# Performance work log

Measured on AMD Instinct MI355X. Metric: run time of the kernel, lower is better.

Reference implementation:

```python
import jax, jax.numpy as jnp
import numpy as np

P, B, D, H, O = 512, 8, 256, 75, 128  # passage_len, batch, input_size, attn hidden, GRU hidden


def setup_inputs() -> dict:
    key = jax.random.key(0)
    ks = jax.random.split(key, 10)

    def w(k, shape, fan_in):
        return jax.random.normal(k, shape, jnp.float32) * (1.0 / np.sqrt(fan_in))

    return {
        "v": jax.random.normal(ks[0], (P, B, D), jnp.float32),
        "Wvp1": w(ks[1], (H, D), D),          # nn.Linear(input_size, hidden, bias=False)
        "Wvp2": w(ks[2], (H, D), D),
        "vw": w(ks[3], (H,), H),               # nn.Linear(hidden, 1, bias=False)
        "Wg": w(ks[4], (2 * D, 2 * D), 2 * D),  # Gate linear, no bias
        "w_ih_f": w(ks[5], (3 * O, 2 * D), 2 * D),
        "w_hh_f": w(ks[6], (3 * O, O), O),
        "b_ih_f": jnp.zeros((3 * O,), jnp.float32),
        "b_hh_f": jnp.zeros((3 * O,), jnp.float32),
        "w_ih_b": w(ks[7], (3 * O, 2 * D), 2 * D),
        "w_hh_b": w(ks[8], (3 * O, O), O),
        "b_ih_b": jnp.zeros((3 * O,), jnp.float32),
        "b_hh_b": jnp.zeros((3 * O,), jnp.float32),
    }


def _gru(x, w_ih, w_hh, b_ih, b_hh):
    # x: (T, B, in) -> hidden states (T, B, O); PyTorch GRU gate order (r, z, n)
    hdim = w_hh.shape[1]
    xp = x @ w_ih.T + b_ih  # precompute input projections: (T, B, 3O)

    def step(h, xp_t):
        gh = h @ w_hh.T + b_hh
        i_r, i_z, i_n = jnp.split(xp_t, 3, axis=-1)
        h_r, h_z, h_n = jnp.split(gh, 3, axis=-1)
        r = jax.nn.sigmoid(i_r + h_r)
        z = jax.nn.sigmoid(i_z + h_z)
        n = jnp.tanh(i_n + r * h_n)
        h_new = (1.0 - z) * n + z * h
        return h_new, h_new

    h0 = jnp.zeros((x.shape[1], hdim), x.dtype)
    _, hs = jax.lax.scan(step, h0, xp)
    return hs


def reference(v, Wvp1, Wvp2, vw, Wg,
              w_ih_f, w_hh_f, b_ih_f, b_hh_f,
              w_ih_b, w_hh_b, b_ih_b, b_hh_b):
    # dropout is inference no-op (and in the torch code its result is discarded anyway)
    Wv1 = v @ Wvp1.T  # (P, B, H) -- broadcast over key axis (dim 1 after expand)
    Wv2 = v @ Wvp2.T  # (P, B, H) -- broadcast over query axis
    # s[i, j, b, h] = tanh(Wv2[i] + Wv1[j]); softmax over i (keys)
    s = jnp.tanh(Wv2[:, None] + Wv1[None, :])          # (P, P, B, H)
    scores = jnp.einsum('ijbh,h->ijb', s, vw)          # (P, P, B)
    a = jax.nn.softmax(scores, axis=0)
    c = jnp.einsum('ijb,ibd->jbd', a, v)               # attended context (P, B, D)
    g = jnp.concatenate([v, c], axis=2)                # (P, B, 2D)
    g = jax.nn.sigmoid(g @ Wg.T) * g                   # Gate
    hf = _gru(g, w_ih_f, w_hh_f, b_ih_f, b_hh_f)
    hb = _gru(g[::-1], w_ih_b, w_hh_b, b_ih_b, b_hh_b)[::-1]
    return jnp.concatenate([hf, hb], axis=2)           # (P, B, 2O)
```

## Files before the change

### kernel.cpp

```cpp
#include <hip/hip_runtime.h>

#define TP 512
#define TB 8
#define TD 256
#define TH 75
#define THP 80
#define TO 128

typedef _Float16 half_t;
typedef _Float16 half2v __attribute__((ext_vector_type(2)));
typedef _Float16 half4v __attribute__((ext_vector_type(4)));
typedef _Float16 half8v __attribute__((ext_vector_type(8)));
typedef float    float4v __attribute__((ext_vector_type(4)));

__device__ __forceinline__ float fast_rcp(float x) { return __builtin_amdgcn_rcpf(x); }
__device__ __forceinline__ float fast_tanh(float x) {
    return 1.0f - 2.0f * fast_rcp(1.0f + __expf(2.0f * x));
}
__device__ __forceinline__ float fast_sigmoid(float x) {
    return fast_rcp(1.0f + __expf(-x));
}
__device__ __forceinline__ float fdot2h(half2v a, half2v b, float c) {
#if __has_builtin(__builtin_amdgcn_fdot2)
    return __builtin_amdgcn_fdot2(a, b, c, false);
#else
    return c + (float)a[0] * (float)b[0] + (float)a[1] * (float)b[1];
#endif
}
#define EXT2(v, j) __builtin_shufflevector((v), (v), 2*(j), 2*(j)+1)
__device__ __forceinline__ void dot3_h8(half8v wr, half8v wz, half8v wn, half8v h,
                                        float& ar, float& az, float& an) {
    half2v h0 = EXT2(h, 0), h1 = EXT2(h, 1), h2 = EXT2(h, 2), h3 = EXT2(h, 3);
    ar = fdot2h(EXT2(wr, 0), h0, ar);
    az = fdot2h(EXT2(wz, 0), h0, az);
    an = fdot2h(EXT2(wn, 0), h0, an);
    ar = fdot2h(EXT2(wr, 1), h1, ar);
    az = fdot2h(EXT2(wz, 1), h1, az);
    an = fdot2h(EXT2(wn, 1), h1, an);
    ar = fdot2h(EXT2(wr, 2), h2, ar);
    az = fdot2h(EXT2(wz, 2), h2, az);
    an = fdot2h(EXT2(wn, 2), h2, an);
    ar = fdot2h(EXT2(wr, 3), h3, ar);
    az = fdot2h(EXT2(wz, 3), h3, az);
    an = fdot2h(EXT2(wn, 3), h3, an);
}
__device__ __forceinline__ float pair_sum_dpp(float v) {
    int i1 = __builtin_amdgcn_update_dpp(0, __builtin_bit_cast(int, v), 0xB1, 0xF, 0xF, true);
    return v + __builtin_bit_cast(float, i1);
}

__global__ __launch_bounds__(256) void prep_kernel(
    const float* __restrict__ v,
    const float* __restrict__ Wvp1, const float* __restrict__ Wvp2,
    const float* __restrict__ Wg,   const float* __restrict__ wihf,
    const float* __restrict__ wihb, const float* __restrict__ bihf,
    const float* __restrict__ bihb, const float* __restrict__ whhf,
    const float* __restrict__ whhb,
    float* __restrict__ bihC,
    half_t* __restrict__ v16, half_t* __restrict__ g16,
    half_t* __restrict__ Wg16B, half_t* __restrict__ Wih16B,
    half_t* __restrict__ whh16, half_t* __restrict__ WT16B)
{
    int idx = blockIdx.x * 256 + threadIdx.x;
    if (idx < 1048576) {
        half_t val = (half_t)v[idx];
        v16[idx] = val;
        int row = idx >> 8, d = idx & 255;
        g16[row * 512 + d] = val;
        return;
    }
    idx -= 1048576;
    if (idx < 768) { bihC[idx] = (idx < 384) ? bihf[idx] : bihb[idx - 384]; return; }
    idx -= 768;
    if (idx < 262144) {
        int j = idx & 7, lane = (idx >> 3) & 63, kt = (idx >> 9) & 15, nt = idx >> 13;
        int o = nt * 16 + (lane & 15);
        int k = kt * 32 + ((lane >> 4) << 3) + j;
        Wg16B[idx] = (half_t)Wg[o * 512 + k];
        return;
    }
    idx -= 262144;
    if (idx < 393216) {
        int j = idx & 7, lane = (idx >> 3) & 63, kt = (idx >> 9) & 15, nt = idx >> 13;
        int o = nt * 16 + (lane & 15);
        int k = kt * 32 + ((lane >> 4) << 3) + j;
        Wih16B[idx] = (half_t)((o < 384) ? wihf[o * 512 + k] : wihb[(o - 384) * 512 + k]);
        return;
    }
    idx -= 393216;
    if (idx < 98304) {
        int d = idx / 49152, i = idx - d * 49152;
        whh16[idx] = (half_t)(d ? whhb[i] : whhf[i]);
        return;
    }
    idx -= 98304;
    if (idx < 40960) {
        int j = idx & 7, lane = (idx >> 3) & 63, kt = (idx >> 9) & 7, nt = idx >> 12;
        int o = nt * 16 + (lane & 15);
        int k = kt * 32 + ((lane >> 4) << 3) + j;
        float vv = 0.0f;
        if (o < 75)       vv = Wvp1[o * 256 + k];
        else if (o < 150) vv = Wvp2[(o - 75) * 256 + k];
        WT16B[idx] = (half_t)vv;
    }
}

__global__ __launch_bounds__(256) void vtrans_kernel(
    const float* __restrict__ v, half_t* __restrict__ vT16)
{
    __shared__ half_t lt[64 * 66];
    int t = threadIdx.x;
    int b  = blockIdx.x >> 5;
    int pt = (blockIdx.x >> 2) & 7;
    int dt = blockIdx.x & 3;

    {
        int pl = t >> 2, dseg = (t & 3) * 16;
        const float4* src = (const float4*)(v + (((pt * 64 + pl) * 8 + b) << 8) + dt * 64 + dseg);
        float4 f0 = src[0], f1 = src[1], f2 = src[2], f3 = src[3];
        half_t hv[16] = {
            (half_t)f0.x,(half_t)f0.y,(half_t)f0.z,(half_t)f0.w,
            (half_t)f1.x,(half_t)f1.y,(half_t)f1.z,(half_t)f1.w,
            (half_t)f2.x,(half_t)f2.y,(half_t)f2.z,(half_t)f2.w,
            (half_t)f3.x,(half_t)f3.y,(half_t)f3.z,(half_t)f3.w };
#pragma unroll
        for (int u = 0; u < 16; ++u) lt[(dseg + u) * 66 + pl] = hv[u];
    }
    __syncthreads();
    {
        int dl = t >> 2, pseg = (t & 3) * 16;
        half8v h0 = *(const half8v*)(lt + dl * 66 + pseg);
        half8v h1 = *(const half8v*)(lt + dl * 66 + pseg + 8);
        half8v* dst = (half8v*)(vT16 + ((b * 256 + dt * 64 + dl) << 9) + pt * 64 + pseg);
        dst[0] = h0; dst[1] = h1;
    }
}

__global__ __launch_bounds__(256) void wv12_kernel(
    const half_t* __restrict__ v16, const half_t* __restrict__ WT16B,
    float* __restrict__ Wv1, float* __restrict__ Wv2T)
{
    int tid = threadIdx.x;
    int lane = tid & 63, w = tid >> 6;
    int l15 = lane & 15, quad = lane >> 4;
    int r0 = blockIdx.x * 64 + w * 16;

    float4v acc[10];
#pragma unroll
    for (int nt = 0; nt < 10; ++nt) acc[nt] = (float4v){0.f, 0.f, 0.f, 0.f};

#pragma unroll
    for (int kt = 0; kt < 8; ++kt) {
        half8v a = *(const half8v*)(v16 + (r0 + l15) * 256 + kt * 32 + quad * 8);
#pragma unroll
        for (int nt = 0; nt < 10; ++nt) {
            half8v b = *(const half8v*)(WT16B + ((nt * 8 + kt) * 64 + lane) * 8);
            acc[nt] = __builtin_amdgcn_mfma_f32_16x16x32_f16(a, b, acc[nt], 0, 0, 0);
        }
    }
#pragma unroll
    for (int nt = 0; nt < 10; ++nt) {
        int col = nt * 16 + l15;
#pragma unroll
        for (int r = 0; r < 4; ++r) {
            int row = r0 + quad * 4 + r;
            int p = row >> 3, b = row & 7;
            int ob = (b * TP + p) * THP;
            float val2 = 2.0f * acc[nt][r];
            if (col < 75)       Wv1[ob + col] = val2;
            else if (col < 80)  { Wv1[ob + col] = 0.0f;
                                  Wv2T[(b * THP + col - 75) * TP + p] = val2; }
            else if (col < 150) Wv2T[(b * THP + col - 75) * TP + p] = val2;
            else if (col < 155) Wv2T[(b * THP + col - 75) * TP + p] = 0.0f;
        }
    }
}

__global__ __launch_bounds__(256) void score_kernel(
    const float* __restrict__ Wv1, const float* __restrict__ Wv2T,
    const float* __restrict__ vw, half_t* __restrict__ a16)
{
    int tid = threadIdx.x;
    int b  = blockIdx.x >> 7;
    int j0 = (blockIdx.x & 127) * 4;
    __shared__ float wv1j[4 * THP];
    __shared__ float vws[THP];
    __shared__ float sc[4 * TP];

    if (tid < THP) vws[tid] = (tid < TH) ? vw[tid] : 0.0f;
    for (int e = tid; e < 4 * THP; e += 256) {
        int jj = e / THP, k = e - jj * THP;
        wv1j[e] = Wv1[(b * TP + j0 + jj) * THP + k];
    }
    __syncthreads();

    float Csum = 0.0f;
    {
        const float4* c4 = (const float4*)vws;
        for (int kk = 0; kk < 20; ++kk) { float4 c = c4[kk]; Csum += c.x + c.y + c.z + c.w; }
    }

    int i0 = tid, i1 = tid + 256;
    float acc0[4] = {0.f,0.f,0.f,0.f}, acc1[4] = {0.f,0.f,0.f,0.f};
    const float* wvt = Wv2T + b * THP * TP;
#pragma unroll
    for (int kt = 0; kt < 5; ++kt) {
        float r0v[16], r1v[16];
#pragma unroll
        for (int u = 0; u < 16; ++u) {
            const float* colp = wvt + (kt * 16 + u) * TP;
            r0v[u] = colp[i0];
            r1v[u] = colp[i1];
        }
        const float* cp = vws + kt * 16;
#pragma unroll
        for (int jj = 0; jj < 4; ++jj) {
            const float* w1 = wv1j + jj * THP + kt * 16;
            float s0 = 0.f, s1 = 0.f;
#pragma unroll
            for (int u = 0; u < 16; ++u) {
                float cu = cp[u], wu = w1[u];
                s0 += cu * fast_rcp(1.0f + __expf(r0v[u] + wu));
                s1 += cu * fast_rcp(1.0f + __expf(r1v[u] + wu));
            }
            acc0[jj] += s0; acc1[jj] += s1;
        }
    }
#pragma unroll
    for (int jj = 0; jj < 4; ++jj) {
        sc[jj * TP + i0] = Csum - 2.0f * acc0[jj];
        sc[jj * TP + i1] = Csum - 2.0f * acc1[jj];
    }
    __syncthreads();

    {
        int jj = tid >> 6, l = tid & 63;
        float m = -1e30f;
#pragma unroll
        for (int q = 0; q < 8; ++q) m = fmaxf(m, sc[jj * TP + l + q * 64]);
#pragma unroll
        for (int s = 32; s > 0; s >>= 1) m = fmaxf(m, __shfl_xor(m, s));
        float e[8];
        float sum = 0.0f;
#pragma unroll
        for (int q = 0; q < 8; ++q) { e[q] = __expf(sc[jj * TP + l + q * 64] - m); sum += e[q]; }
#pragma unroll
        for (int s = 32; s > 0; s >>= 1) sum += __shfl_xor(sum, s);
        float inv = fast_rcp(sum);
        half_t* arow = a16 + (b * TP + j0 + jj) * TP;
#pragma unroll
        for (int q = 0; q < 8; ++q) arow[l + q * 64] = (half_t)(e[q] * inv);
    }
}

__global__ __launch_bounds__(256) void context_kernel(
    const half_t* __restrict__ a16, const half_t* __restrict__ vT16,
    half_t* __restrict__ g16)
{
    int tid = threadIdx.x;
    int lane = tid & 63, w = tid >> 6;
    int l15 = lane & 15, quad = lane >> 4;
    int b  = blockIdx.x >> 5;
    int mt = blockIdx.x & 31;

    const half_t* arow = a16 + (b * TP + mt * 16 + l15) * TP;
    const half_t* vbase = vT16 + ((b * 256) << 9);

    float4v acc[4];
#pragma unroll
    for (int nti = 0; nti < 4; ++nti) acc[nti] = (float4v){0.f, 0.f, 0.f, 0.f};

#pragma unroll 4
    for (int kt = 0; kt < 16; ++kt) {
        half8v a = *(const half8v*)(arow + kt * 32 + quad * 8);
#pragma unroll
        for (int nti = 0; nti < 4; ++nti) {
            int d = (w * 4 + nti) * 16 + l15;
            half8v bb = *(const half8v*)(vbase + (d << 9) + kt * 32 + quad * 8);
            acc[nti] = __builtin_amdgcn_mfma_f32_16x16x32_f16(a, bb, acc[nti], 0, 0, 0);
        }
    }
#pragma unroll
    for (int nti = 0; nti < 4; ++nti) {
        int d = (w * 4 + nti) * 16 + l15;
#pragma unroll
        for (int r = 0; r < 4; ++r) {
            int j = mt * 16 + quad * 4 + r;
            g16[(j * TB + b) * 512 + 256 + d] = (half_t)acc[nti][r];
        }
    }
}

__global__ __launch_bounds__(256, 1) void gatexp_kernel(
    const half_t* __restrict__ g16, const half_t* __restrict__ Wg16B,
    const half_t* __restrict__ Wih16B, const float* __restrict__ bihC,
    float* __restrict__ xpf, float* __restrict__ xpb)
{
    __shared__ half_t gA[32 * 520];
    int tid = threadIdx.x;
    int r0 = blockIdx.x * 32;
    int lane = tid & 63, w = tid >> 6;
    int l15 = lane & 15, quad = lane >> 4;

    for (int e = tid; e < 2048; e += 256) {
        int row = e >> 6, c8 = e & 63;
        *(half8v*)(gA + row * 520 + c8 * 8) =
            *(const half8v*)(g16 + (r0 + row) * 512 + c8 * 8);
    }
    __syncthreads();

    float4v acc[2][8];
#pragma unroll
    for (int mi = 0; mi < 2; ++mi)
#pragma unroll
        for (int nti = 0; nti < 8; ++nti) acc[mi][nti] = (float4v){0.f, 0.f, 0.f, 0.f};

    for (int kt = 0; kt < 16; ++kt) {
        half8v a0 = *(const half8v*)(gA + l15 * 520 + kt * 32 + quad * 8);
        half8v a1 = *(const half8v*)(gA + (16 + l15) * 520 + kt * 32 + quad * 8);
#pragma unroll
        for (int nti = 0; nti < 8; ++nti) {
            half8v bb = *(const half8v*)(Wg16B + (((w * 8 + nti) * 16 + kt) * 64 + lane) * 8);
            acc[0][nti] = __builtin_amdgcn_mfma_f32_16x16x32_f16(a0, bb, acc[0][nti], 0, 0, 0);
            acc[1][nti] = __builtin_amdgcn_mfma_f32_16x16x32_f16(a1, bb, acc[1][nti], 0, 0, 0);
        }
    }
#pragma unroll
    for (int mi = 0; mi < 2; ++mi)
#pragma unroll
        for (int nti = 0; nti < 8; ++nti) {
            int colg = (w * 8 + nti) * 16 + l15;
#pragma unroll
            for (int r = 0; r < 4; ++r) {
                float gv = (float)gA[(mi * 16 + quad * 4 + r) * 520 + colg];
                acc[mi][nti][r] = fast_sigmoid(acc[mi][nti][r]) * gv;
            }
        }
    __syncthreads();
#pragma unroll
    for (int mi = 0; mi < 2; ++mi)
#pragma unroll
        for (int nti = 0; nti < 8; ++nti) {
            int colg = (w * 8 + nti) * 16 + l15;
#pragma unroll
            for (int r = 0; r < 4; ++r)
                gA[(mi * 16 + quad * 4 + r) * 520 + colg] = (half_t)acc[mi][nti][r];
        }
    __syncthreads();

    float4v c2[2][12];
#pragma unroll
    for (int mi = 0; mi < 2; ++mi)
#pragma unroll
        for (int nt2 = 0; nt2 < 12; ++nt2) {
            float bv = bihC[(w * 12 + nt2) * 16 + l15];
            c2[mi][nt2] = (float4v){bv, bv, bv, bv};
        }

    for (int kt = 0; kt < 16; ++kt) {
        half8v a0 = *(const half8v*)(gA + l15 * 520 + kt * 32 + quad * 8);
        half8v a1 = *(const half8v*)(gA + (16 + l15) * 520 + kt * 32 + quad * 8);
#pragma unroll
        for (int nt2 = 0; nt2 < 12; ++nt2) {
            half8v bb = *(const half8v*)(Wih16B + (((w * 12 + nt2) * 16 + kt) * 64 + lane) * 8);
            c2[0][nt2] = __builtin_amdgcn_mfma_f32_16x16x32_f16(a0, bb, c2[0][nt2], 0, 0, 0);
            c2[1][nt2] = __builtin_amdgcn_mfma_f32_16x16x32_f16(a1, bb, c2[1][nt2], 0, 0, 0);
        }
    }
#pragma unroll
    for (int mi = 0; mi < 2; ++mi)
#pragma unroll
        for (int nt2 = 0; nt2 < 12; ++nt2) {
            int col = (w * 12 + nt2) * 16 + l15;
            float* dst = (col < 384) ? (xpf + col) : (xpb + col - 384);
#pragma unroll
            for (int r = 0; r < 4; ++r)
                dst[(r0 + mi * 16 + quad * 4 + r) * 384] = c2[mi][nt2][r];
        }
}

__global__ __launch_bounds__(256, 1) void gru_kernel(
    const float* __restrict__ xpf, const float* __restrict__ xpb,
    const half_t* __restrict__ whh16,
    const float* __restrict__ bhhf, const float* __restrict__ bhhb,
    float* __restrict__ out)
{
    int tid = threadIdx.x;
    int dir = blockIdx.x >> 3;
    int b   = blockIdx.x & 7;
    const float* xp  = dir ? xpb  : xpf;
    const float* bhh = dir ? bhhb : bhhf;
    const half_t* wbase = whh16 + dir * 3 * TO * TO;

    __shared__ __align__(16) half_t hb[2][TO];

    int o = tid >> 1, hf = tid & 1;

    half8v wr[8], wz[8], wn[8];
    {
        const half_t* pr = wbase + (o)          * TO + hf * 64;
        const half_t* pz = wbase + (TO + o)     * TO + hf * 64;
        const half_t* pn = wbase + (2 * TO + o) * TO + hf * 64;
        asm volatile(
            "global_load_dwordx4 %0,  %24, off\n\t"
            "global_load_dwordx4 %1,  %24, off offset:16\n\t"
            "global_load_dwordx4 %2,  %24, off offset:32\n\t"
            "global_load_dwordx4 %3,  %24, off offset:48\n\t"
            "global_load_dwordx4 %4,  %24, off offset:64\n\t"
            "global_load_dwordx4 %5,  %24, off offset:80\n\t"
            "global_load_dwordx4 %6,  %24, off offset:96\n\t"
            "global_load_dwordx4 %7,  %24, off offset:112\n\t"
            "global_load_dwordx4 %8,  %25, off\n\t"
            "global_load_dwordx4 %9,  %25, off offset:16\n\t"
            "global_load_dwordx4 %10, %25, off offset:32\n\t"
            "global_load_dwordx4 %11, %25, off offset:48\n\t"
            "global_load_dwordx4 %12, %25, off offset:64\n\t"
            "global_load_dwordx4 %13, %25, off offset:80\n\t"
            "global_load_dwordx4 %14, %25, off offset:96\n\t"
            "global_load_dwordx4 %15, %25, off offset:112\n\t"
            "global_load_dwordx4 %16, %26, off\n\t"
            "global_load_dwordx4 %17, %26, off offset:16\n\t"
            "global_load_dwordx4 %18, %26, off offset:32\n\t"
            "global_load_dwordx4 %19, %26, off offset:48\n\t"
            "global_load_dwordx4 %20, %26, off offset:64\n\t"
            "global_load_dwordx4 %21, %26, off offset:80\n\t"
            "global_load_dwordx4 %22, %26, off offset:96\n\t"
            "global_load_dwordx4 %23, %26, off offset:112\n\t"
            "s_waitcnt vmcnt(0)"
            : "=&v"(wr[0]), "=&v"(wr[1]), "=&v"(wr[2]), "=&v"(wr[3]),
              "=&v"(wr[4]), "=&v"(wr[5]), "=&v"(wr[6]), "=&v"(wr[7]),
              "=&v"(wz[0]), "=&v"(wz[1]), "=&v"(wz[2]), "=&v"(wz[3]),
              "=&v"(wz[4]), "=&v"(wz[5]), "=&v"(wz[6]), "=&v"(wz[7]),
              "=&v"(wn[0]), "=&v"(wn[1]), "=&v"(wn[2]), "=&v"(wn[3]),
              "=&v"(wn[4]), "=&v"(wn[5]), "=&v"(wn[6]), "=&v"(wn[7])
            : "v"(pr), "v"(pz), "v"(pn));
    }

    float br = 0.f, bz = 0.f, bn = 0.f, h = 0.f;
    if (hf == 0) {
        br = bhh[o]; bz = bhh[TO + o]; bn = bhh[2 * TO + o];
    }
    if (tid < TO) hb[0][tid] = (half_t)0.0f;
    __syncthreads();

    float xrv[8], xzv[8], xnv[8], hist[8];

    for (int S = 0; S < TP; S += 8) {
        if (hf == 0) {
#pragma unroll
            for (int u = 0; u < 8; ++u) {
                int s = S + u;
                int tn = dir ? (TP - 1 - s) : s;
                const float* xpt = xp + (tn * TB + b) * 384;
                xrv[u] = xpt[o]; xzv[u] = xpt[TO + o]; xnv[u] = xpt[2 * TO + o];
            }
        }
#pragma unroll
        for (int u = 0; u < 8; ++u) {
            int s = S + u;
            int cur = s & 1;
            const half8v* h8 = (const half8v*)(&hb[cur][hf * 64]);
            half8v hv0 = h8[0], hv1 = h8[1], hv2 = h8[2], hv3 = h8[3];
            half8v hv4 = h8[4], hv5 = h8[5], hv6 = h8[6], hv7 = h8[7];

            float ar = 0.f, az = 0.f, an = 0.f;
            dot3_h8(wr[0], wz[0], wn[0], hv0, ar, az, an);
            dot3_h8(wr[1], wz[1], wn[1], hv1, ar, az, an);
            dot3_h8(wr[2], wz[2], wn[2], hv2, ar, az, an);
            dot3_h8(wr[3], wz[3], wn[3], hv3, ar, az, an);
            dot3_h8(wr[4], wz[4], wn[4], hv4, ar, az, an);
            dot3_h8(wr[5], wz[5], wn[5], hv5, ar, az, an);
            dot3_h8(wr[6], wz[6], wn[6], hv6, ar, az, an);
            dot3_h8(wr[7], wz[7], wn[7], hv7, ar, az, an);

            ar = pair_sum_dpp(ar);
            az = pair_sum_dpp(az);
            an = pair_sum_dpp(an);
            if (hf == 0) {
                float r = fast_sigmoid(xrv[u] + ar + br);
                float z = fast_sigmoid(xzv[u] + az + bz);
                float n = fast_tanh(xnv[u] + r * (an + bn));
                h = (1.0f - z) * n + z * h;
                hb[cur ^ 1][o] = (half_t)h;
                hist[u] = h;
            }
            __syncthreads();
        }
        if (hf == 0) {
#pragma unroll
            for (int u = 0; u < 8; ++u) {
                int s = S + u;
                int t = dir ? (TP - 1 - s) : s;
                out[(t * TB + b) * 256 + dir * TO + o] = hist[u];
            }
        }
    }
}

extern "C" void kernel_launch(void* const* d_in, const int* in_sizes, int n_in,
                              void* d_out, int out_size, void* d_ws, size_t ws_size,
                              hipStream_t stream) {
    const float* v    = (const float*)d_in[0];
    const float* Wvp1 = (const float*)d_in[1];
    const float* Wvp2 = (const float*)d_in[2];
    const float* vw   = (const float*)d_in[3];
    const float* Wg   = (const float*)d_in[4];
    const float* wihf = (const float*)d_in[5];
    const float* whhf = (const float*)d_in[6];
    const float* bihf = (const float*)d_in[7];
    const float* bhhf = (const float*)d_in[8];
    const float* wihb = (const float*)d_in[9];
    const float* whhb = (const float*)d_in[10];
    const float* bihb = (const float*)d_in[11];
    const float* bhhb = (const float*)d_in[12];

    float* ws   = (float*)d_ws;
    float* bihC = ws;
    float* Wv1  = bihC + 768;
    float* Wv2T = Wv1 + 327680;
    float* xpf  = Wv2T + 327680;
    float* xpb  = xpf + 1572864;
    half_t* g16    = (half_t*)(xpb + 1572864);
    half_t* Wg16B  = g16 + 2097152;
    half_t* Wih16B = Wg16B + 262144;
    half_t* whh16  = Wih16B + 393216;
    half_t* v16    = whh16 + 98304;
    half_t* WT16B  = v16 + 1048576;
    half_t* vT16   = WT16B + 40960;
    half_t* a16    = vT16 + 1048576;
    float* out  = (float*)d_out;

    prep_kernel<<<7203, 256, 0, stream>>>(v, Wvp1, Wvp2, Wg, wihf, wihb, bihf, bihb,
                                          whhf, whhb, bihC, v16, g16,
                                          Wg16B, Wih16B, whh16, WT16B);
    vtrans_kernel<<<256, 256, 0, stream>>>(v, vT16);
    wv12_kernel<<<64, 256, 0, stream>>>(v16, WT16B, Wv1, Wv2T);
    score_kernel<<<1024, 256, 0, stream>>>(Wv1, Wv2T, vw, a16);
    context_kernel<<<256, 256, 0, stream>>>(a16, vT16, g16);
    gatexp_kernel<<<128, 256, 0, stream>>>(g16, Wg16B, Wih16B, bihC, xpf, xpb);
    gru_kernel<<<16, 256, 0, stream>>>(xpf, xpb, whh16, bhhf, bhhb, out);
}
```

Measured before the change: 435.1 us.

## Fold exp2 scaling into GRU weights, prefetch projections, split dot-product chains

Prescales the GRU input and hidden weights and biases by -log2(e) or 2*log2(e), so sigmoid and tanh become a single native exp2 plus a reciprocal. The input projections and biases are folded into the dot-product accumulators as initial values. It also splits each accumulation into two independent chains to shorten the dependency path, and prefetches the next 8 steps of input projections a block ahead. The intent is to cut latency in the serial GRU recurrence, at the cost of scaling weights before the fp16 cast, which slightly changes rounding.

```diff
diff --git a/kernel.cpp b/kernel.cpp
--- a/kernel.cpp
+++ b/kernel.cpp
@@ -7,6 +7,9 @@
 #define THP 80
 #define TO 128
 
+#define SCRZ (-1.4426950408889634f)
+#define SCN  ( 2.8853900817779268f)
+
 typedef _Float16 half_t;
 typedef _Float16 half2v __attribute__((ext_vector_type(2)));
 typedef _Float16 half4v __attribute__((ext_vector_type(4)));
@@ -14,6 +17,13 @@
 typedef float    float4v __attribute__((ext_vector_type(4)));
 
 __device__ __forceinline__ float fast_rcp(float x) { return __builtin_amdgcn_rcpf(x); }
+__device__ __forceinline__ float ex2(float x) {
+#if __has_builtin(__builtin_amdgcn_exp2f)
+    return __builtin_amdgcn_exp2f(x);
+#else
+    float r; asm("v_exp_f32 %0, %1" : "=v"(r) : "v"(x)); return r;
+#endif
+}
 __device__ __forceinline__ float fast_tanh(float x) {
     return 1.0f - 2.0f * fast_rcp(1.0f + __expf(2.0f * x));
 }
@@ -70,7 +80,12 @@
         return;
     }
     idx -= 1048576;
-    if (idx < 768) { bihC[idx] = (idx < 384) ? bihf[idx] : bihb[idx - 384]; return; }
+    if (idx < 768) {
+        int c = (idx < 384) ? idx : idx - 384;
+        float sc = ((c >> 7) == 2) ? SCN : SCRZ;
+        bihC[idx] = sc * ((idx < 384) ? bihf[idx] : bihb[idx - 384]);
+        return;
+    }
     idx -= 768;
     if (idx < 262144) {
         int j = idx & 7, lane = (idx >> 3) & 63, kt = (idx >> 9) & 15, nt = idx >> 13;
@@ -84,13 +99,17 @@
         int j = idx & 7, lane = (idx >> 3) & 63, kt = (idx >> 9) & 15, nt = idx >> 13;
         int o = nt * 16 + (lane & 15);
         int k = kt * 32 + ((lane >> 4) << 3) + j;
-        Wih16B[idx] = (half_t)((o < 384) ? wihf[o * 512 + k] : wihb[(o - 384) * 512 + k]);
+        float wv_ = (o < 384) ? wihf[o * 512 + k] : wihb[(o - 384) * 512 + k];
+        int og = ((o < 384) ? o : o - 384) >> 7;
+        float sc = (og == 2) ? SCN : SCRZ;
+        Wih16B[idx] = (half_t)(wv_ * sc);
         return;
     }
     idx -= 393216;
     if (idx < 98304) {
         int d = idx / 49152, i = idx - d * 49152;
-        whh16[idx] = (half_t)(d ? whhb[i] : whhf[i]);
+        float sc = ((i >> 14) == 2) ? SCN : SCRZ;
+        whh16[idx] = (half_t)(sc * (d ? whhb[i] : whhf[i]));
         return;
     }
     idx -= 98304;
@@ -438,21 +457,37 @@
 
     float br = 0.f, bz = 0.f, bn = 0.f, h = 0.f;
     if (hf == 0) {
-        br = bhh[o]; bz = bhh[TO + o]; bn = bhh[2 * TO + o];
+        br = SCRZ * bhh[o]; bz = SCRZ * bhh[TO + o]; bn = SCN * bhh[2 * TO + o];
     }
     if (tid < TO) hb[0][tid] = (half_t)0.0f;
     __syncthreads();
 
     float xrv[8], xzv[8], xnv[8], hist[8];
+    float nxr[8], nxz[8], nxn[8];
+
+    if (hf == 0) {
+#pragma unroll
+        for (int u = 0; u < 8; ++u) {
+            int tn = dir ? (TP - 1 - u) : u;
+            const float* xpt = xp + (tn * TB + b) * 384;
+            nxr[u] = xpt[o]; nxz[u] = xpt[TO + o]; nxn[u] = xpt[2 * TO + o];
+        }
+    }
 
     for (int S = 0; S < TP; S += 8) {
         if (hf == 0) {
 #pragma unroll
             for (int u = 0; u < 8; ++u) {
-                int s = S + u;
-                int tn = dir ? (TP - 1 - s) : s;
-                const float* xpt = xp + (tn * TB + b) * 384;
-                xrv[u] = xpt[o]; xzv[u] = xpt[TO + o]; xnv[u] = xpt[2 * TO + o];
+                xrv[u] = nxr[u] + br; xzv[u] = nxz[u] + bz; xnv[u] = nxn[u];
+            }
+            if (S + 8 < TP) {
+#pragma unroll
+                for (int u = 0; u < 8; ++u) {
+                    int s = S + 8 + u;
+                    int tn = dir ? (TP - 1 - s) : s;
+                    const float* xpt = xp + (tn * TB + b) * 384;
+                    nxr[u] = xpt[o]; nxz[u] = xpt[TO + o]; nxn[u] = xpt[2 * TO + o];
+                }
             }
         }
 #pragma unroll
@@ -463,24 +498,27 @@
             half8v hv0 = h8[0], hv1 = h8[1], hv2 = h8[2], hv3 = h8[3];
             half8v hv4 = h8[4], hv5 = h8[5], hv6 = h8[6], hv7 = h8[7];
 
-            float ar = 0.f, az = 0.f, an = 0.f;
-            dot3_h8(wr[0], wz[0], wn[0], hv0, ar, az, an);
-            dot3_h8(wr[1], wz[1], wn[1], hv1, ar, az, an);
-            dot3_h8(wr[2], wz[2], wn[2], hv2, ar, az, an);
-            dot3_h8(wr[3], wz[3], wn[3], hv3, ar, az, an);
-            dot3_h8(wr[4], wz[4], wn[4], hv4, ar, az, an);
-            dot3_h8(wr[5], wz[5], wn[5], hv5, ar, az, an);
-            dot3_h8(wr[6], wz[6], wn[6], hv6, ar, az, an);
-            dot3_h8(wr[7], wz[7], wn[7], hv7, ar, az, an);
-
-            ar = pair_sum_dpp(ar);
-            az = pair_sum_dpp(az);
-            an = pair_sum_dpp(an);
+            float ar0 = (hf == 0) ? xrv[u] : 0.f;
+            float az0 = (hf == 0) ? xzv[u] : 0.f;
+            float an0 = (hf == 0) ? bn     : 0.f;
+            float ar1 = 0.f, az1 = 0.f, an1 = 0.f;
+            dot3_h8(wr[0], wz[0], wn[0], hv0, ar0, az0, an0);
+            dot3_h8(wr[1], wz[1], wn[1], hv1, ar0, az0, an0);
+            dot3_h8(wr[2], wz[2], wn[2], hv2, ar0, az0, an0);
+            dot3_h8(wr[3], wz[3], wn[3], hv3, ar0, az0, an0);
+            dot3_h8(wr[4], wz[4], wn[4], hv4, ar1, az1, an1);
+            dot3_h8(wr[5], wz[5], wn[5], hv5, ar1, az1, an1);
+            dot3_h8(wr[6], wz[6], wn[6], hv6, ar1, az1, an1);
+            dot3_h8(wr[7], wz[7], wn[7], hv7, ar1, az1, an1);
+
+            float ar = pair_sum_dpp(ar0 + ar1);
+            float az = pair_sum_dpp(az0 + az1);
+            float an = pair_sum_dpp(an0 + an1);
             if (hf == 0) {
-                float r = fast_sigmoid(xrv[u] + ar + br);
-                float z = fast_sigmoid(xzv[u] + az + bz);
-                float n = fast_tanh(xnv[u] + r * (an + bn));
-                h = (1.0f - z) * n + z * h;
+                float r = fast_rcp(1.0f + ex2(ar));
+                float z = fast_rcp(1.0f + ex2(az));
+                float n = 1.0f - 2.0f * fast_rcp(1.0f + ex2(xnv[u] + r * an));
+                h = n + z * (h - n);
                 hb[cur ^ 1][o] = (half_t)h;
                 hist[u] = h;
             }
```

New measurement: 454.5 us. 1.04x slower.
